# Optimization experiments

Hardware: AMD Instinct MI355X
Metric: run time of the kernel (lower is better)

Reference implementation:

```python
import jax, jax.numpy as jnp
import numpy as np

B, IN_DIM, HID, OUT_DIM, K = 16384, 400, 24, 4096, 64


def setup_inputs() -> dict:
    key = jax.random.key(0)
    ks = jax.random.split(key, 20)
    bnd = 1.0 / np.sqrt(IN_DIM)

    def factorized_eps(k, shape):
        # sign(x)*sqrt(|x|) of small gaussian noise, outer-product factorized
        if len(shape) == 2:
            ko, ki = jax.random.split(k)
            eo = jax.random.normal(ko, (shape[0],)) * 0.001
            ei = jax.random.normal(ki, (shape[1],)) * 0.001
            f = lambda v: jnp.sign(v) * jnp.sqrt(jnp.abs(v))
            return jnp.outer(f(eo), f(ei))
        e = jax.random.normal(k, shape) * 0.001
        return jnp.sign(e) * jnp.sqrt(jnp.abs(e))

    sig2 = 0.5 / np.sqrt(HID)
    sig3 = 0.5 / np.sqrt(OUT_DIM)
    bnd24 = 1.0 / np.sqrt(HID)
    return {
        "x": jax.random.normal(ks[0], (B, IN_DIM), dtype=jnp.float32),
        "possible_moves": jax.random.randint(ks[1], (B, K), 0, OUT_DIM),
        "W1": jax.random.uniform(ks[2], (HID, IN_DIM), minval=-bnd, maxval=bnd),
        "b1": jax.random.uniform(ks[3], (HID,), minval=-bnd, maxval=bnd),
        "mu_w2": jax.random.uniform(ks[4], (HID, HID), minval=-bnd24, maxval=bnd24),
        "mu_b2": jax.random.uniform(ks[5], (HID,), minval=-bnd24, maxval=bnd24),
        "sigma_w2": jnp.full((HID, HID), sig2, dtype=jnp.float32),
        "sigma_b2": jnp.full((HID,), sig2, dtype=jnp.float32),
        "eps_w2": factorized_eps(ks[6], (HID, HID)),
        "eps_b2": factorized_eps(ks[7], (HID,)),
        "mu_w3": jax.random.uniform(ks[8], (OUT_DIM, HID), minval=-bnd24, maxval=bnd24),
        "mu_b3": jax.random.uniform(ks[9], (OUT_DIM,), minval=-bnd24, maxval=bnd24),
        "sigma_w3": jnp.full((OUT_DIM, HID), sig3, dtype=jnp.float32),
        "sigma_b3": jnp.full((OUT_DIM,), sig3, dtype=jnp.float32),
        "eps_w3": factorized_eps(ks[10], (OUT_DIM, HID)),
        "eps_b3": factorized_eps(ks[11], (OUT_DIM,)),
    }


def reference(x, possible_moves, W1, b1, mu_w2, mu_b2, sigma_w2, sigma_b2,
              eps_w2, eps_b2, mu_w3, mu_b3, sigma_w3, sigma_b3, eps_w3, eps_b3):
    h = jax.nn.relu(x @ W1.T + b1)
    w2 = mu_w2 + sigma_w2 * eps_w2
    h = jax.nn.relu(h @ w2.T + (mu_b2 + sigma_b2 * eps_b2))
    w3 = mu_w3 + sigma_w3 * eps_w3
    logits = h @ w3.T + (mu_b3 + sigma_b3 * eps_b3)  # [B, OUT_DIM]
    # scatter 1.0 at legal-move indices per row (vectorized LegalSoftmax)
    rows = jnp.arange(logits.shape[0])[:, None]
    mask = jnp.zeros(logits.shape, logits.dtype).at[rows, possible_moves].set(1.0)
    filtered = logits * mask
    return jnp.where(filtered == 0, -jnp.inf, filtered)
```

## Files before the change

### kernel.cpp

```cpp
#include <hip/hip_runtime.h>
#include <math.h>

#define BATCH 16384
#define IN_DIM 400
#define HID 24
#define OUT_DIM 4096
#define KMOV 64

#define SENT_BITS 0xFF7F0000u

__global__ __launch_bounds__(256) void precompute_w3(
    const float* __restrict__ mu_w3, const float* __restrict__ sigma_w3,
    const float* __restrict__ eps_w3, const float* __restrict__ mu_b3,
    const float* __restrict__ sigma_b3, const float* __restrict__ eps_b3,
    float* __restrict__ w3eff, float* __restrict__ b3eff) {
    const int stride = gridDim.x * blockDim.x;
    for (int i = blockIdx.x * blockDim.x + threadIdx.x; i < OUT_DIM * HID; i += stride)
        w3eff[i] = mu_w3[i] + sigma_w3[i] * eps_w3[i];
    for (int i = blockIdx.x * blockDim.x + threadIdx.x; i < OUT_DIM; i += stride)
        b3eff[i] = mu_b3[i] + sigma_b3[i] * eps_b3[i];
}

__global__ __launch_bounds__(256) void noisy_fused_pre(
    const float* __restrict__ x, const int* __restrict__ moves,
    const float* __restrict__ W1, const float* __restrict__ b1,
    const float* __restrict__ mu_w2, const float* __restrict__ mu_b2,
    const float* __restrict__ sigma_w2, const float* __restrict__ sigma_b2,
    const float* __restrict__ eps_w2, const float* __restrict__ eps_b2,
    const float* __restrict__ w3eff, const float* __restrict__ b3eff,
    float* __restrict__ out) {
    __shared__ float w2s[HID * HID];
    __shared__ float b2s[HID];
    __shared__ float h1s[HID];
    __shared__ float h2s[HID];

    const int tid = threadIdx.x;
    const int lane = tid & 63;
    const int wave = tid >> 6;
    const int row = blockIdx.x;
    const float SENT = __uint_as_float(SENT_BITS);

    const float4 n4 = make_float4(SENT, SENT, SENT, SENT);
    float4* orow = (float4*)(out + (size_t)row * OUT_DIM);
#pragma unroll
    for (int i = 0; i < 4; ++i) orow[i * 256 + tid] = n4;

    int idx = 0;
    if (tid < KMOV) idx = moves[(size_t)row * KMOV + tid];

    for (int i = tid; i < HID * HID; i += 256)
        w2s[i] = mu_w2[i] + sigma_w2[i] * eps_w2[i];
    if (tid < HID) b2s[tid] = mu_b2[tid] + sigma_b2[tid] * eps_b2[tid];

    {
        const float4* xv = (const float4*)(x + (size_t)row * IN_DIM);
        const float4* w1v = (const float4*)W1;
        float4 xa = xv[lane];
        float4 xb = make_float4(0.f, 0.f, 0.f, 0.f);
        const bool hasB = (lane < IN_DIM / 4 - 64);
        if (hasB) xb = xv[64 + lane];

#pragma unroll
        for (int t = 0; t < 6; ++t) {
            const int u = wave * 6 + t;
            const float4* wrow = w1v + u * (IN_DIM / 4);
            float4 wa = wrow[lane];
            float acc = xa.x * wa.x + xa.y * wa.y + xa.z * wa.z + xa.w * wa.w;
            if (hasB) {
                float4 wb = wrow[64 + lane];
                acc += xb.x * wb.x + xb.y * wb.y + xb.z * wb.z + xb.w * wb.w;
            }
            acc += __shfl_xor(acc, 32);
            acc += __shfl_xor(acc, 16);
            acc += __shfl_xor(acc, 8);
            acc += __shfl_xor(acc, 4);
            acc += __shfl_xor(acc, 2);
            acc += __shfl_xor(acc, 1);
            if (lane == 0) h1s[u] = fmaxf(acc + b1[u], 0.f);
        }
    }
    __syncthreads();

    if (tid < HID) {
        float acc = b2s[tid];
#pragma unroll
        for (int j = 0; j < HID; ++j) acc += h1s[j] * w2s[tid * HID + j];
        h2s[tid] = fmaxf(acc, 0.f);
    }
    __syncthreads();

    if (tid < KMOV) {
        float acc = b3eff[idx];
        const float4* wr = (const float4*)(w3eff + idx * HID);
#pragma unroll
        for (int q = 0; q < 6; ++q) {
            float4 w4 = wr[q];
            acc += h2s[q * 4 + 0] * w4.x + h2s[q * 4 + 1] * w4.y +
                   h2s[q * 4 + 2] * w4.z + h2s[q * 4 + 3] * w4.w;
        }
        float val = (acc != 0.f) ? acc : SENT;
        out[(size_t)row * OUT_DIM + idx] = val;
    }
}

__global__ __launch_bounds__(256) void noisy_fused_fly(
    const float* __restrict__ x, const int* __restrict__ moves,
    const float* __restrict__ W1, const float* __restrict__ b1,
    const float* __restrict__ mu_w2, const float* __restrict__ mu_b2,
    const float* __restrict__ sigma_w2, const float* __restrict__ sigma_b2,
    const float* __restrict__ eps_w2, const float* __restrict__ eps_b2,
    const float* __restrict__ mu_w3, const float* __restrict__ mu_b3,
    const float* __restrict__ sigma_w3, const float* __restrict__ sigma_b3,
    const float* __restrict__ eps_w3, const float* __restrict__ eps_b3,
    float* __restrict__ out) {
    __shared__ float w2s[HID * HID];
    __shared__ float b2s[HID];
    __shared__ float h1s[HID];
    __shared__ float h2s[HID];

    const int tid = threadIdx.x;
    const int lane = tid & 63;
    const int wave = tid >> 6;
    const int row = blockIdx.x;
    const float SENT = __uint_as_float(SENT_BITS);

    const float4 n4 = make_float4(SENT, SENT, SENT, SENT);
    float4* orow = (float4*)(out + (size_t)row * OUT_DIM);
#pragma unroll
    for (int i = 0; i < 4; ++i) orow[i * 256 + tid] = n4;

    int idx = 0;
    if (tid < KMOV) idx = moves[(size_t)row * KMOV + tid];

    for (int i = tid; i < HID * HID; i += 256)
        w2s[i] = mu_w2[i] + sigma_w2[i] * eps_w2[i];
    if (tid < HID) b2s[tid] = mu_b2[tid] + sigma_b2[tid] * eps_b2[tid];

    {
        const float4* xv = (const float4*)(x + (size_t)row * IN_DIM);
        const float4* w1v = (const float4*)W1;
        float4 xa = xv[lane];
        float4 xb = make_float4(0.f, 0.f, 0.f, 0.f);
        const bool hasB = (lane < IN_DIM / 4 - 64);
        if (hasB) xb = xv[64 + lane];
#pragma unroll
        for (int t = 0; t < 6; ++t) {
            const int u = wave * 6 + t;
            const float4* wrow = w1v + u * (IN_DIM / 4);
            float4 wa = wrow[lane];
            float acc = xa.x * wa.x + xa.y * wa.y + xa.z * wa.z + xa.w * wa.w;
            if (hasB) {
                float4 wb = wrow[64 + lane];
                acc += xb.x * wb.x + xb.y * wb.y + xb.z * wb.z + xb.w * wb.w;
            }
            acc += __shfl_xor(acc, 32);
            acc += __shfl_xor(acc, 16);
            acc += __shfl_xor(acc, 8);
            acc += __shfl_xor(acc, 4);
            acc += __shfl_xor(acc, 2);
            acc += __shfl_xor(acc, 1);
            if (lane == 0) h1s[u] = fmaxf(acc + b1[u], 0.f);
        }
    }
    __syncthreads();

    if (tid < HID) {
        float acc = b2s[tid];
#pragma unroll
        for (int j = 0; j < HID; ++j) acc += h1s[j] * w2s[tid * HID + j];
        h2s[tid] = fmaxf(acc, 0.f);
    }
    __syncthreads();

    if (tid < KMOV) {
        float acc = mu_b3[idx] + sigma_b3[idx] * eps_b3[idx];
        const float4* mr = (const float4*)(mu_w3 + idx * HID);
        const float4* sr = (const float4*)(sigma_w3 + idx * HID);
        const float4* er = (const float4*)(eps_w3 + idx * HID);
#pragma unroll
        for (int q = 0; q < 6; ++q) {
            float4 m4 = mr[q], s4 = sr[q], e4 = er[q];
            acc += h2s[q * 4 + 0] * (m4.x + s4.x * e4.x) +
                   h2s[q * 4 + 1] * (m4.y + s4.y * e4.y) +
                   h2s[q * 4 + 2] * (m4.z + s4.z * e4.z) +
                   h2s[q * 4 + 3] * (m4.w + s4.w * e4.w);
        }
        float val = (acc != 0.f) ? acc : SENT;
        out[(size_t)row * OUT_DIM + idx] = val;
    }
}

extern "C" void kernel_launch(void* const* d_in, const int* in_sizes, int n_in,
                              void* d_out, int out_size, void* d_ws, size_t ws_size,
                              hipStream_t stream) {
    const float* x        = (const float*)d_in[0];
    const int*   moves    = (const int*)d_in[1];
    const float* W1       = (const float*)d_in[2];
    const float* b1       = (const float*)d_in[3];
    const float* mu_w2    = (const float*)d_in[4];
    const float* mu_b2    = (const float*)d_in[5];
    const float* sigma_w2 = (const float*)d_in[6];
    const float* sigma_b2 = (const float*)d_in[7];
    const float* eps_w2   = (const float*)d_in[8];
    const float* eps_b2   = (const float*)d_in[9];
    const float* mu_w3    = (const float*)d_in[10];
    const float* mu_b3    = (const float*)d_in[11];
    const float* sigma_w3 = (const float*)d_in[12];
    const float* sigma_b3 = (const float*)d_in[13];
    const float* eps_w3   = (const float*)d_in[14];
    const float* eps_b3   = (const float*)d_in[15];
    float* out = (float*)d_out;

    float* w3eff = (float*)d_ws;
    float* b3eff = w3eff + OUT_DIM * HID;
    const size_t need = (size_t)(OUT_DIM * HID + OUT_DIM) * sizeof(float);

    if (ws_size >= need) {
        precompute_w3<<<256, 256, 0, stream>>>(mu_w3, sigma_w3, eps_w3,
                                               mu_b3, sigma_b3, eps_b3,
                                               w3eff, b3eff);
        noisy_fused_pre<<<BATCH, 256, 0, stream>>>(
            x, moves, W1, b1, mu_w2, mu_b2, sigma_w2, sigma_b2, eps_w2, eps_b2,
            w3eff, b3eff, out);
    } else {
        noisy_fused_fly<<<BATCH, 256, 0, stream>>>(
            x, moves, W1, b1, mu_w2, mu_b2, sigma_w2, sigma_b2, eps_w2, eps_b2,
            mu_w3, mu_b3, sigma_w3, sigma_b3, eps_w3, eps_b3, out);
    }
}
```

Measured before the change: 432.7 us.

## Split logits compute from output fill; merge scattered logits via shared row buffer

The fused per-row kernel becomes two kernels. compute_logits writes 64 compacted logits per row to workspace, and fill_merge builds each 4096-wide output row in LDS (sentinel fill plus scatter) and writes it out with coalesced float4 stores. This replaces the scattered global writes that followed the sentinel fill. W2/b2 folding also moves into the precompute kernel. The cost is an extra kernel launch, a workspace round-trip for the logits, and more workspace, and the new path runs only if the workspace is large enough.

```diff
diff --git a/kernel.cpp b/kernel.cpp
--- a/kernel.cpp
+++ b/kernel.cpp
@@ -9,26 +9,37 @@
 
 #define SENT_BITS 0xFF7F0000u
 
-__global__ __launch_bounds__(256) void precompute_w3(
+#define WS_W3   0
+#define WS_B3   (WS_W3 + OUT_DIM * HID)
+#define WS_W2   (WS_B3 + OUT_DIM)
+#define WS_B2   (WS_W2 + HID * HID)
+#define WS_LOG  (WS_B2 + HID)
+#define WS_NEED ((size_t)(WS_LOG + BATCH * KMOV) * sizeof(float))
+
+__global__ __launch_bounds__(256) void precompute_folds(
+    const float* __restrict__ mu_w2, const float* __restrict__ mu_b2,
+    const float* __restrict__ sigma_w2, const float* __restrict__ sigma_b2,
+    const float* __restrict__ eps_w2, const float* __restrict__ eps_b2,
     const float* __restrict__ mu_w3, const float* __restrict__ sigma_w3,
     const float* __restrict__ eps_w3, const float* __restrict__ mu_b3,
     const float* __restrict__ sigma_b3, const float* __restrict__ eps_b3,
-    float* __restrict__ w3eff, float* __restrict__ b3eff) {
+    float* __restrict__ ws) {
     const int stride = gridDim.x * blockDim.x;
-    for (int i = blockIdx.x * blockDim.x + threadIdx.x; i < OUT_DIM * HID; i += stride)
-        w3eff[i] = mu_w3[i] + sigma_w3[i] * eps_w3[i];
-    for (int i = blockIdx.x * blockDim.x + threadIdx.x; i < OUT_DIM; i += stride)
-        b3eff[i] = mu_b3[i] + sigma_b3[i] * eps_b3[i];
-}
-
-__global__ __launch_bounds__(256) void noisy_fused_pre(
+    const int g = blockIdx.x * blockDim.x + threadIdx.x;
+    for (int i = g; i < OUT_DIM * HID; i += stride)
+        ws[WS_W3 + i] = mu_w3[i] + sigma_w3[i] * eps_w3[i];
+    for (int i = g; i < OUT_DIM; i += stride)
+        ws[WS_B3 + i] = mu_b3[i] + sigma_b3[i] * eps_b3[i];
+    for (int i = g; i < HID * HID; i += stride)
+        ws[WS_W2 + i] = mu_w2[i] + sigma_w2[i] * eps_w2[i];
+    for (int i = g; i < HID; i += stride)
+        ws[WS_B2 + i] = mu_b2[i] + sigma_b2[i] * eps_b2[i];
+}
+
+__global__ __launch_bounds__(256) void compute_logits(
     const float* __restrict__ x, const int* __restrict__ moves,
     const float* __restrict__ W1, const float* __restrict__ b1,
-    const float* __restrict__ mu_w2, const float* __restrict__ mu_b2,
-    const float* __restrict__ sigma_w2, const float* __restrict__ sigma_b2,
-    const float* __restrict__ eps_w2, const float* __restrict__ eps_b2,
-    const float* __restrict__ w3eff, const float* __restrict__ b3eff,
-    float* __restrict__ out) {
+    float* __restrict__ ws) {
     __shared__ float w2s[HID * HID];
     __shared__ float b2s[HID];
     __shared__ float h1s[HID];
@@ -40,17 +51,11 @@
     const int row = blockIdx.x;
     const float SENT = __uint_as_float(SENT_BITS);
 
-    const float4 n4 = make_float4(SENT, SENT, SENT, SENT);
-    float4* orow = (float4*)(out + (size_t)row * OUT_DIM);
-#pragma unroll
-    for (int i = 0; i < 4; ++i) orow[i * 256 + tid] = n4;
-
     int idx = 0;
     if (tid < KMOV) idx = moves[(size_t)row * KMOV + tid];
 
-    for (int i = tid; i < HID * HID; i += 256)
-        w2s[i] = mu_w2[i] + sigma_w2[i] * eps_w2[i];
-    if (tid < HID) b2s[tid] = mu_b2[tid] + sigma_b2[tid] * eps_b2[tid];
+    for (int i = tid; i < HID * HID; i += 256) w2s[i] = ws[WS_W2 + i];
+    if (tid < HID) b2s[tid] = ws[WS_B2 + tid];
 
     {
         const float4* xv = (const float4*)(x + (size_t)row * IN_DIM);
@@ -90,17 +95,42 @@
     __syncthreads();
 
     if (tid < KMOV) {
-        float acc = b3eff[idx];
-        const float4* wr = (const float4*)(w3eff + idx * HID);
+        float acc = ws[WS_B3 + idx];
+        const float4* wr = (const float4*)(ws + WS_W3 + idx * HID);
 #pragma unroll
         for (int q = 0; q < 6; ++q) {
             float4 w4 = wr[q];
             acc += h2s[q * 4 + 0] * w4.x + h2s[q * 4 + 1] * w4.y +
                    h2s[q * 4 + 2] * w4.z + h2s[q * 4 + 3] * w4.w;
         }
-        float val = (acc != 0.f) ? acc : SENT;
-        out[(size_t)row * OUT_DIM + idx] = val;
-    }
+        ws[WS_LOG + (size_t)row * KMOV + tid] = (acc != 0.f) ? acc : SENT;
+    }
+}
+
+__global__ __launch_bounds__(256) void fill_merge(
+    const int* __restrict__ moves, const float* __restrict__ ws,
+    float* __restrict__ out) {
+    __shared__ float rowbuf[OUT_DIM];
+
+    const int tid = threadIdx.x;
+    const int row = blockIdx.x;
+    const float SENT = __uint_as_float(SENT_BITS);
+    const float4 n4 = make_float4(SENT, SENT, SENT, SENT);
+
+    float4* rb4 = (float4*)rowbuf;
+#pragma unroll
+    for (int i = 0; i < 4; ++i) rb4[i * 256 + tid] = n4;
+    __syncthreads();
+
+    if (tid < KMOV) {
+        const int idx = moves[(size_t)row * KMOV + tid];
+        rowbuf[idx] = ws[WS_LOG + (size_t)row * KMOV + tid];
+    }
+    __syncthreads();
+
+    float4* orow = (float4*)(out + (size_t)row * OUT_DIM);
+#pragma unroll
+    for (int i = 0; i < 4; ++i) orow[i * 256 + tid] = rb4[i * 256 + tid];
 }
 
 __global__ __launch_bounds__(256) void noisy_fused_fly(
@@ -185,8 +215,7 @@
                    h2s[q * 4 + 2] * (m4.z + s4.z * e4.z) +
                    h2s[q * 4 + 3] * (m4.w + s4.w * e4.w);
         }
-        float val = (acc != 0.f) ? acc : SENT;
-        out[(size_t)row * OUT_DIM + idx] = val;
+        out[(size_t)row * OUT_DIM + idx] = (acc != 0.f) ? acc : SENT;
     }
 }
 
@@ -210,18 +239,14 @@
     const float* eps_w3   = (const float*)d_in[14];
     const float* eps_b3   = (const float*)d_in[15];
     float* out = (float*)d_out;
-
-    float* w3eff = (float*)d_ws;
-    float* b3eff = w3eff + OUT_DIM * HID;
-    const size_t need = (size_t)(OUT_DIM * HID + OUT_DIM) * sizeof(float);
-
-    if (ws_size >= need) {
-        precompute_w3<<<256, 256, 0, stream>>>(mu_w3, sigma_w3, eps_w3,
-                                               mu_b3, sigma_b3, eps_b3,
-                                               w3eff, b3eff);
-        noisy_fused_pre<<<BATCH, 256, 0, stream>>>(
-            x, moves, W1, b1, mu_w2, mu_b2, sigma_w2, sigma_b2, eps_w2, eps_b2,
-            w3eff, b3eff, out);
+    float* ws  = (float*)d_ws;
+
+    if (ws_size >= WS_NEED) {
+        precompute_folds<<<256, 256, 0, stream>>>(
+            mu_w2, mu_b2, sigma_w2, sigma_b2, eps_w2, eps_b2,
+            mu_w3, sigma_w3, eps_w3, mu_b3, sigma_b3, eps_b3, ws);
+        compute_logits<<<BATCH, 256, 0, stream>>>(x, moves, W1, b1, ws);
+        fill_merge<<<BATCH, 256, 0, stream>>>(moves, ws, out);
     } else {
         noisy_fused_fly<<<BATCH, 256, 0, stream>>>(
             x, moves, W1, b1, mu_w2, mu_b2, sigma_w2, sigma_b2, eps_w2, eps_b2,
```

After: 383.0 us. 11.5% less time.
